# Kernel tuning notes

Measured on AMD Instinct MI355X. Metric: run time of the kernel, lower is better.

The kernel has to match this reference:

```python
import jax, jax.numpy as jnp
import numpy as np

K = 6
D_IN = 128
D_OUT = 128
N_COARSE = 4000
N_FINE = 40000


def setup_inputs() -> dict:
    key = jax.random.key(0)
    k1, k2, k3, k4, k5 = jax.random.split(key, 5)
    x_coarse = jax.random.normal(k1, (N_COARSE, D_IN), dtype=jnp.float32)
    pos_coarse = jax.random.uniform(k2, (N_COARSE, 3), dtype=jnp.float32)
    pos_fine = jax.random.uniform(k3, (N_FINE, 3), dtype=jnp.float32)
    # nnx.Linear params: lecun_normal kernel, zero bias (use small random for generality)
    W = jax.random.normal(k4, (D_IN, D_OUT), dtype=jnp.float32) / np.sqrt(D_IN)
    b = jax.random.normal(k5, (D_OUT,), dtype=jnp.float32) * 0.01
    return {"x_coarse": x_coarse, "pos_coarse": pos_coarse, "pos_fine": pos_fine, "W": W, "b": b}


def reference(x_coarse, pos_coarse, pos_fine, W, b):
    # dense pairwise L2 distances [Nf, Nc] (faithful to the original's full matrix)
    distances = jnp.linalg.norm(pos_fine[:, None, :] - pos_coarse[None, :, :], axis=-1)
    # full argsort then slice, matching the original (incl. tie-break order)
    knn_idx = jnp.argsort(distances, axis=1)[:, :K]        # [Nf, K]
    gathered = x_coarse[knn_idx]                            # [Nf, K, d_in]
    interp = jnp.mean(gathered, axis=1)                     # [Nf, d_in]
    return interp @ W + b                                   # [Nf, d_out]
```

## Files before the change

### kernel.cpp

```cpp
#include <hip/hip_runtime.h>
#include <cstdint>

#define NCOARSE 4000
#define NFINE   40000
#define DIM     128
#define GRES    8
#define CELLH   0.125f
#define FCAP    384
#define NB_B    128
#define NB_Y    125
#define NBUILD  (NB_B + NB_Y)

__device__ __forceinline__ uint64_t min64(uint64_t a, uint64_t b) { return a < b ? a : b; }
__device__ __forceinline__ uint64_t max64(uint64_t a, uint64_t b) { return a > b ? a : b; }
__device__ __forceinline__ int cell_coord(float x) {
    int c = (int)(x * 8.0f);
    return c < 0 ? 0 : (c > 7 ? 7 : c);
}

union BuildSM {
    uint16_t cellS[4096];
    float    xs[32][DIM];
};

__global__ __launch_bounds__(256) void k_build(const float* __restrict__ pc,
                                               const float* __restrict__ xc,
                                               const float* __restrict__ W,
                                               int*    __restrict__ nbrCnt,
                                               float4* __restrict__ flatC,
                                               float*  __restrict__ Y) {
    __shared__ BuildSM sm;
    const int bid = blockIdx.x, tid = threadIdx.x;

    if (bid < NB_B) {
        #pragma unroll
        for (int t = 0; t < 16; ++t) {
            const int idx = t * 256 + tid;
            uint16_t cv = 0xFFFF;
            if (idx < NCOARSE)
                cv = (uint16_t)((cell_coord(pc[3*idx+2]) << 6) |
                                (cell_coord(pc[3*idx+1]) << 3) |
                                 cell_coord(pc[3*idx]));
            sm.cellS[idx] = cv;
        }
        __syncthreads();
        const int wid = tid >> 6, lane = tid & 63;
        const int hc = bid * 4 + wid;
        const int hx = hc & 7, hy = (hc >> 3) & 7, hz = hc >> 6;
        const int bx0 = max(hx-1,0), bx1 = min(hx+1,7);
        const int by0 = max(hy-1,0), by1 = min(hy+1,7);
        const int bz0 = max(hz-1,0), bz1 = min(hz+1,7);
        int off = 0;
        for (int it = 0; it < 63; ++it) {
            const int j = it * 64 + lane;
            const uint16_t cid = sm.cellS[j];
            const int cx = cid & 7, cy = (cid >> 3) & 7, cz = cid >> 6;
            const bool in = (j < NCOARSE) && cx >= bx0 && cx <= bx1 &&
                            cy >= by0 && cy <= by1 && cz >= bz0 && cz <= bz1;
            const unsigned long long mask = __ballot(in);
            if (in) {
                const int d = off + (int)__popcll(mask & ((1ull << lane) - 1ull));
                if (d < FCAP)
                    flatC[hc * FCAP + d] =
                        make_float4(pc[3*j], pc[3*j+1], pc[3*j+2], __int_as_float(j));
            }
            off += (int)__popcll(mask);
        }
        if (lane == 0) nbrCnt[hc] = off;
    } else {
        const int g  = bid - NB_B;
        const int r0 = g * 32;
        #pragma unroll
        for (int t = 0; t < 4; ++t)
            reinterpret_cast<float4*>(sm.xs)[tid + t * 256] =
                reinterpret_cast<const float4*>(xc + r0 * DIM)[tid + t * 256];
        __syncthreads();
        const int rq = tid >> 5;
        const int jq = tid & 31;
        float acc[4][4];
        #pragma unroll
        for (int i = 0; i < 4; ++i)
            #pragma unroll
            for (int j = 0; j < 4; ++j) acc[i][j] = 0.f;
        #pragma unroll 2
        for (int k = 0; k < DIM; ++k) {
            const float4 wv = *reinterpret_cast<const float4*>(W + k * DIM + jq * 4);
            #pragma unroll
            for (int i = 0; i < 4; ++i) {
                const float a = sm.xs[rq + 8 * i][k];
                acc[i][0] += a * wv.x; acc[i][1] += a * wv.y;
                acc[i][2] += a * wv.z; acc[i][3] += a * wv.w;
            }
        }
        #pragma unroll
        for (int i = 0; i < 4; ++i)
            *reinterpret_cast<float4*>(Y + (r0 + rq + 8 * i) * DIM + jq * 4) =
                make_float4(acc[i][0], acc[i][1], acc[i][2], acc[i][3]);
    }
}

__device__ __forceinline__ void popmin_merge(const uint64_t own[7], uint64_t mg[7]) {
    uint64_t a0 = own[0], a1 = own[1], a2 = own[2], a3 = own[3],
             a4 = own[4], a5 = own[5], a6 = own[6];
    #pragma unroll
    for (int r = 0; r < 7; ++r) {
        uint64_t m = a0;
        m = min64(m, __shfl_xor((unsigned long long)m, 1));
        m = min64(m, __shfl_xor((unsigned long long)m, 2));
        m = min64(m, __shfl_xor((unsigned long long)m, 4));
        mg[r] = m;
        const bool win = (a0 == m);
        a0 = win ? a1 : a0;
        a1 = win ? a2 : a1;
        a2 = win ? a3 : a2;
        a3 = win ? a4 : a3;
        a4 = win ? a5 : a4;
        a5 = win ? a6 : a5;
        a6 = win ? ~0ull : a6;
    }
}

__device__ __forceinline__ bool done_check(uint64_t k7, float fx, float fy, float fz,
                                           int ix, int iy, int iz, int s) {
    const float d7 = __uint_as_float((uint32_t)(k7 >> 32));
    float clear = 1e30f;
    if (ix - s >= 0) clear = fminf(clear, __fsub_rn(fx, (float)(ix - s) * CELLH));
    if (ix + s <= 6) clear = fminf(clear, __fsub_rn((float)(ix + s + 1) * CELLH, fx));
    if (iy - s >= 0) clear = fminf(clear, __fsub_rn(fy, (float)(iy - s) * CELLH));
    if (iy + s <= 6) clear = fminf(clear, __fsub_rn((float)(iy + s + 1) * CELLH, fy));
    if (iz - s >= 0) clear = fminf(clear, __fsub_rn(fz, (float)(iz - s) * CELLH));
    if (iz + s <= 6) clear = fminf(clear, __fsub_rn((float)(iz + s + 1) * CELLH, fz));
    return d7 < clear * clear * 0.9999f;
}

#define INS(p) { \
    const float ddx = __fsub_rn(fx, (p).x); \
    const float ddy = __fsub_rn(fy, (p).y); \
    const float ddz = __fsub_rn(fz, (p).z); \
    const float d2  = __fadd_rn(__fadd_rn(__fmul_rn(ddx, ddx), __fmul_rn(ddy, ddy)), \
                                __fmul_rn(ddz, ddz)); \
    const uint64_t v = ((uint64_t)__float_as_uint(d2) << 32) | (uint32_t)__float_as_uint((p).w); \
    if (v < own[6]) { \
        own[6] = min64(own[6], max64(own[5], v)); \
        own[5] = min64(own[5], max64(own[4], v)); \
        own[4] = min64(own[4], max64(own[3], v)); \
        own[3] = min64(own[3], max64(own[2], v)); \
        own[2] = min64(own[2], max64(own[1], v)); \
        own[1] = min64(own[1], max64(own[0], v)); \
        own[0] = min64(own[0], v); \
    } }

#define BRUTE() { \
    _Pragma("unroll") \
    for (int r = 0; r < 7; ++r) own[r] = ~0ull; \
    for (int i = par; i < NCOARSE; i += 8) { \
        const float4 p = make_float4(pc[3*i], pc[3*i+1], pc[3*i+2], __int_as_float(i)); \
        INS(p) \
    } }

__global__ __launch_bounds__(256) void k_main(
    const float*  __restrict__ Y,
    const float*  __restrict__ bias,
    const int*    __restrict__ nbrCnt,
    const float4* __restrict__ flatC,
    const float*  __restrict__ pc,
    const float*  __restrict__ pf,
    float* __restrict__ out)
{
    const int tid = threadIdx.x;
    const int fl  = tid >> 3;
    const int par = tid & 7;
    const int f   = blockIdx.x * 32 + fl;

    const float fx = pf[3*f], fy = pf[3*f+1], fz = pf[3*f+2];
    const int ix = cell_coord(fx), iy = cell_coord(fy), iz = cell_coord(fz);
    const int cell = (iz << 6) | (iy << 3) | ix;

    const int total = nbrCnt[cell];

    uint64_t own[7];
    #pragma unroll
    for (int r = 0; r < 7; ++r) own[r] = ~0ull;
    uint64_t mg[7];

    if (total <= FCAP) {
        const float4* fpts = flatC + cell * FCAP;
        #pragma unroll 2
        for (int i = par; i < total; i += 8) { const float4 p = fpts[i]; INS(p) }
        popmin_merge(own, mg);
        if (!done_check(mg[6], fx, fy, fz, ix, iy, iz, 1)) {
            BRUTE();
            popmin_merge(own, mg);
        }
    } else {
        BRUTE();
        popmin_merge(own, mg);
    }

    int i5 = (int)(uint32_t)mg[5];
    {
        const int i6 = (int)(uint32_t)mg[6];
        const float d5 = sqrtf(__uint_as_float((uint32_t)(mg[5] >> 32)));
        const float d6 = sqrtf(__uint_as_float((uint32_t)(mg[6] >> 32)));
        if (d5 == d6 && i6 < i5) i5 = i6;
    }
    const int id0 = (int)(uint32_t)mg[0];
    const int id1 = (int)(uint32_t)mg[1];
    const int id2 = (int)(uint32_t)mg[2];
    const int id3 = (int)(uint32_t)mg[3];
    const int id4 = (int)(uint32_t)mg[4];
    const int id5 = i5;

    constexpr float inv6 = 1.0f / 6.0f;
    #pragma unroll
    for (int k = 0; k < 4; ++k) {
        const int q = (k * 8 + par) * 4;
        const float4 y0 = *reinterpret_cast<const float4*>(Y + id0 * DIM + q);
        const float4 y1 = *reinterpret_cast<const float4*>(Y + id1 * DIM + q);
        const float4 y2 = *reinterpret_cast<const float4*>(Y + id2 * DIM + q);
        const float4 y3 = *reinterpret_cast<const float4*>(Y + id3 * DIM + q);
        const float4 y4 = *reinterpret_cast<const float4*>(Y + id4 * DIM + q);
        const float4 y5 = *reinterpret_cast<const float4*>(Y + id5 * DIM + q);
        const float4 bv = *reinterpret_cast<const float4*>(bias + q);
        float4 o;
        o.x = (y0.x + y1.x + y2.x + y3.x + y4.x + y5.x) * inv6 + bv.x;
        o.y = (y0.y + y1.y + y2.y + y3.y + y4.y + y5.y) * inv6 + bv.y;
        o.z = (y0.z + y1.z + y2.z + y3.z + y4.z + y5.z) * inv6 + bv.z;
        o.w = (y0.w + y1.w + y2.w + y3.w + y4.w + y5.w) * inv6 + bv.w;
        *reinterpret_cast<float4*>(out + f * DIM + q) = o;
    }
}

extern "C" void kernel_launch(void* const* d_in, const int* in_sizes, int n_in,
                              void* d_out, int out_size, void* d_ws, size_t ws_size,
                              hipStream_t stream) {
    const float* xc = (const float*)d_in[0];
    const float* pc = (const float*)d_in[1];
    const float* pf = (const float*)d_in[2];
    const float* W  = (const float*)d_in[3];
    const float* b  = (const float*)d_in[4];
    float* out = (float*)d_out;

    int*    nbrCnt = (int*)d_ws;
    float4* flatC  = (float4*)((char*)d_ws + 4096);
    float*  Y      = (float*)((char*)d_ws + 3149824);

    k_build<<<dim3(NBUILD),      dim3(256), 0, stream>>>(pc, xc, W, nbrCnt, flatC, Y);
    k_main <<<dim3(NFINE / 32),  dim3(256), 0, stream>>>(Y, b, nbrCnt, flatC, pc, pf, out);
}
```

Measured before the change: 51.28 us.

## Sort neighbor candidates by distance to cell center and terminate scan early

The build kernel now sorts each cell's candidate list by distance to the cell center, using a shared-memory rank sort, and stores the sorted distances. The main kernel scans candidates in chunks of 64. It stops once the current 6th-best distance plus the query's offset from the cell center falls below the next candidate's center distance, which is a triangle-inequality bound. This cuts distance evaluations per query, but adds an O(m^2) rank sort to the build, extra shuffles, and a data-dependent loop exit.

Result: slower. 65.63 us (+28.0%).

```diff
diff --git a/kernel.cpp b/kernel.cpp
--- a/kernel.cpp
+++ b/kernel.cpp
@@ -19,8 +19,11 @@
 }
 
 union BuildSM {
-    uint16_t cellS[4096];
-    float    xs[32][DIM];
+    struct {
+        uint16_t cellS[4096];
+        uint64_t keys[4][FCAP];
+    } l;
+    float xs[32][DIM];
 };
 
 __global__ __launch_bounds__(256) void k_build(const float* __restrict__ pc,
@@ -28,6 +31,7 @@
                                                const float* __restrict__ W,
                                                int*    __restrict__ nbrCnt,
                                                float4* __restrict__ flatC,
+                                               float*  __restrict__ dsSorted,
                                                float*  __restrict__ Y) {
     __shared__ BuildSM sm;
     const int bid = blockIdx.x, tid = threadIdx.x;
@@ -41,7 +45,7 @@
                 cv = (uint16_t)((cell_coord(pc[3*idx+2]) << 6) |
                                 (cell_coord(pc[3*idx+1]) << 3) |
                                  cell_coord(pc[3*idx]));
-            sm.cellS[idx] = cv;
+            sm.l.cellS[idx] = cv;
         }
         __syncthreads();
         const int wid = tid >> 6, lane = tid & 63;
@@ -50,23 +54,43 @@
         const int bx0 = max(hx-1,0), bx1 = min(hx+1,7);
         const int by0 = max(hy-1,0), by1 = min(hy+1,7);
         const int bz0 = max(hz-1,0), bz1 = min(hz+1,7);
+        const float ccx = ((float)hx + 0.5f) * CELLH;
+        const float ccy = ((float)hy + 0.5f) * CELLH;
+        const float ccz = ((float)hz + 0.5f) * CELLH;
+
         int off = 0;
         for (int it = 0; it < 63; ++it) {
             const int j = it * 64 + lane;
-            const uint16_t cid = sm.cellS[j];
+            const uint16_t cid = sm.l.cellS[j];
             const int cx = cid & 7, cy = (cid >> 3) & 7, cz = cid >> 6;
             const bool in = (j < NCOARSE) && cx >= bx0 && cx <= bx1 &&
                             cy >= by0 && cy <= by1 && cz >= bz0 && cz <= bz1;
             const unsigned long long mask = __ballot(in);
             if (in) {
                 const int d = off + (int)__popcll(mask & ((1ull << lane) - 1ull));
-                if (d < FCAP)
-                    flatC[hc * FCAP + d] =
-                        make_float4(pc[3*j], pc[3*j+1], pc[3*j+2], __int_as_float(j));
+                if (d < FCAP) {
+                    const float dx = pc[3*j]   - ccx;
+                    const float dy = pc[3*j+1] - ccy;
+                    const float dz = pc[3*j+2] - ccz;
+                    const float d2c = dx*dx + dy*dy + dz*dz;
+                    sm.l.keys[wid][d] = ((uint64_t)__float_as_uint(d2c) << 32) | (uint32_t)j;
+                }
             }
             off += (int)__popcll(mask);
         }
         if (lane == 0) nbrCnt[hc] = off;
+        __syncthreads();
+
+        const int m = min(off, FCAP);
+        for (int l = lane; l < m; l += 64) {
+            const uint64_t k = sm.l.keys[wid][l];
+            int r = 0;
+            for (int q = 0; q < m; ++q) r += (sm.l.keys[wid][q] < k) ? 1 : 0;
+            const int j = (int)(uint32_t)k;
+            flatC[hc * FCAP + r] = make_float4(pc[3*j], pc[3*j+1], pc[3*j+2],
+                                               __int_as_float(j));
+            dsSorted[hc * FCAP + r] = sqrtf(__uint_as_float((uint32_t)(k >> 32)));
+        }
     } else {
         const int g  = bid - NB_B;
         const int r0 = g * 32;
@@ -163,6 +187,7 @@
     const float*  __restrict__ bias,
     const int*    __restrict__ nbrCnt,
     const float4* __restrict__ flatC,
+    const float*  __restrict__ dsSorted,
     const float*  __restrict__ pc,
     const float*  __restrict__ pf,
     float* __restrict__ out)
@@ -176,6 +201,12 @@
     const int ix = cell_coord(fx), iy = cell_coord(fy), iz = cell_coord(fz);
     const int cell = (iz << 6) | (iy << 3) | ix;
 
+    const float ccx = ((float)ix + 0.5f) * CELLH;
+    const float ccy = ((float)iy + 0.5f) * CELLH;
+    const float ccz = ((float)iz + 0.5f) * CELLH;
+    const float rfx = fx - ccx, rfy = fy - ccy, rfz = fz - ccz;
+    const float rf = sqrtf(rfx*rfx + rfy*rfy + rfz*rfz) * 1.0001f + 1e-6f;
+
     const int total = nbrCnt[cell];
 
     uint64_t own[7];
@@ -185,8 +216,21 @@
 
     if (total <= FCAP) {
         const float4* fpts = flatC + cell * FCAP;
-        #pragma unroll 2
-        for (int i = par; i < total; i += 8) { const float4 p = fpts[i]; INS(p) }
+        const float*  dss  = dsSorted + cell * FCAP;
+        int base = 0;
+        while (base < total) {
+            const int lim = min(base + 64, total);
+            for (int i = base + par; i < lim; i += 8) { const float4 p = fpts[i]; INS(p) }
+            base = lim;
+            if (base < total) {
+                uint64_t u7 = own[6];
+                u7 = min64(u7, __shfl_xor((unsigned long long)u7, 1));
+                u7 = min64(u7, __shfl_xor((unsigned long long)u7, 2));
+                u7 = min64(u7, __shfl_xor((unsigned long long)u7, 4));
+                const float d7u = sqrtf(__uint_as_float((uint32_t)(u7 >> 32)));
+                if ((d7u + rf) * 1.0002f < dss[base]) break;
+            }
+        }
         popmin_merge(own, mg);
         if (!done_check(mg[6], fx, fy, fz, ix, iy, iz, 1)) {
             BRUTE();
@@ -241,10 +285,13 @@
     const float* b  = (const float*)d_in[4];
     float* out = (float*)d_out;
 
-    int*    nbrCnt = (int*)d_ws;
-    float4* flatC  = (float4*)((char*)d_ws + 4096);
-    float*  Y      = (float*)((char*)d_ws + 3149824);
-
-    k_build<<<dim3(NBUILD),      dim3(256), 0, stream>>>(pc, xc, W, nbrCnt, flatC, Y);
-    k_main <<<dim3(NFINE / 32),  dim3(256), 0, stream>>>(Y, b, nbrCnt, flatC, pc, pf, out);
-}
+    int*    nbrCnt   = (int*)d_ws;
+    float4* flatC    = (float4*)((char*)d_ws + 4096);
+    float*  dsSorted = (float*)((char*)d_ws + 3149824);
+    float*  Y        = (float*)((char*)d_ws + 3936256);
+
+    k_build<<<dim3(NBUILD),     dim3(256), 0, stream>>>(pc, xc, W, nbrCnt, flatC,
+                                                        dsSorted, Y);
+    k_main <<<dim3(NFINE / 32), dim3(256), 0, stream>>>(Y, b, nbrCnt, flatC, dsSorted,
+                                                        pc, pf, out);
+}
```

## Use 16^3 subcell candidate lists pruned by kNN-radius bound

Applied to the files above, without the earlier changes.

Replaces the per-8^3-cell 27-neighborhood candidate lists (up to 384 points) with per-16^3-subcell lists. Each subcell's list holds only the coarse points within a radius derived from the 7th-nearest distance to the subcell center plus the subcell half-diagonal. The main kernel then scans a much shorter list per fine point and uses a triangle-inequality check against the stored radius to decide whether to fall back to brute force. This costs a heavier build kernel: 1024 build blocks each doing a wave-wide kNN and a filter pass. It also risks more brute-force fallbacks when the bound fails.

After: 48.72 us. 5.0% less time.

```diff
diff --git a/kernel.cpp b/kernel.cpp
--- a/kernel.cpp
+++ b/kernel.cpp
@@ -6,10 +6,13 @@
 #define DIM     128
 #define GRES    8
 #define CELLH   0.125f
-#define FCAP    384
-#define NB_B    128
+#define SUBH    0.0625f
+#define MCAP    384
+#define FCAP2   192
+#define NB_S    1024
 #define NB_Y    125
-#define NBUILD  (NB_B + NB_Y)
+#define NBUILD  (NB_S + NB_Y)
+#define LPP     8
 
 __device__ __forceinline__ uint64_t min64(uint64_t a, uint64_t b) { return a < b ? a : b; }
 __device__ __forceinline__ uint64_t max64(uint64_t a, uint64_t b) { return a > b ? a : b; }
@@ -17,22 +20,31 @@
     int c = (int)(x * 8.0f);
     return c < 0 ? 0 : (c > 7 ? 7 : c);
 }
+__device__ __forceinline__ int cell16(float x) {
+    int c = (int)(x * 16.0f);
+    return c < 0 ? 0 : (c > 15 ? 15 : c);
+}
 
 union BuildSM {
-    uint16_t cellS[4096];
-    float    xs[32][DIM];
+    struct {
+        uint16_t cellS[4096];
+        uint16_t memberIdx[MCAP];
+        int mcount, mflag;
+    } l;
+    float xs[32][DIM];
 };
 
 __global__ __launch_bounds__(256) void k_build(const float* __restrict__ pc,
                                                const float* __restrict__ xc,
                                                const float* __restrict__ W,
                                                int*    __restrict__ nbrCnt,
-                                               float4* __restrict__ flatC,
+                                               float*  __restrict__ Rarr,
+                                               float4* __restrict__ flatS,
                                                float*  __restrict__ Y) {
     __shared__ BuildSM sm;
     const int bid = blockIdx.x, tid = threadIdx.x;
 
-    if (bid < NB_B) {
+    if (bid < NB_S) {
         #pragma unroll
         for (int t = 0; t < 16; ++t) {
             const int idx = t * 256 + tid;
@@ -41,34 +53,120 @@
                 cv = (uint16_t)((cell_coord(pc[3*idx+2]) << 6) |
                                 (cell_coord(pc[3*idx+1]) << 3) |
                                  cell_coord(pc[3*idx]));
-            sm.cellS[idx] = cv;
+            sm.l.cellS[idx] = cv;
         }
         __syncthreads();
+
         const int wid = tid >> 6, lane = tid & 63;
-        const int hc = bid * 4 + wid;
-        const int hx = hc & 7, hy = (hc >> 3) & 7, hz = hc >> 6;
-        const int bx0 = max(hx-1,0), bx1 = min(hx+1,7);
-        const int by0 = max(hy-1,0), by1 = min(hy+1,7);
-        const int bz0 = max(hz-1,0), bz1 = min(hz+1,7);
-        int off = 0;
-        for (int it = 0; it < 63; ++it) {
-            const int j = it * 64 + lane;
-            const uint16_t cid = sm.cellS[j];
-            const int cx = cid & 7, cy = (cid >> 3) & 7, cz = cid >> 6;
-            const bool in = (j < NCOARSE) && cx >= bx0 && cx <= bx1 &&
-                            cy >= by0 && cy <= by1 && cz >= bz0 && cz <= bz1;
+        const int parent = bid >> 1;
+        const int px = parent & 7, py = (parent >> 3) & 7, pz = parent >> 6;
+        const int bx0 = max(px-1,0), bx1 = min(px+1,7);
+        const int by0 = max(py-1,0), by1 = min(py+1,7);
+        const int bz0 = max(pz-1,0), bz1 = min(pz+1,7);
+
+        if (wid == 0) {
+            int off = 0;
+            for (int it = 0; it < 63; ++it) {
+                const int j = it * 64 + lane;
+                const uint16_t cid = sm.l.cellS[j];
+                const int cx = cid & 7, cy = (cid >> 3) & 7, cz = cid >> 6;
+                const bool in = (j < NCOARSE) && cx >= bx0 && cx <= bx1 &&
+                                cy >= by0 && cy <= by1 && cz >= bz0 && cz <= bz1;
+                const unsigned long long mask = __ballot(in);
+                if (in) {
+                    const int d = off + (int)__popcll(mask & ((1ull << lane) - 1ull));
+                    if (d < MCAP) sm.l.memberIdx[d] = (uint16_t)j;
+                }
+                off += (int)__popcll(mask);
+            }
+            if (lane == 0) { sm.l.mcount = min(off, MCAP); sm.l.mflag = (off > MCAP); }
+        }
+        __syncthreads();
+
+        const int  mcount = sm.l.mcount;
+        const bool mflag  = sm.l.mflag != 0;
+
+        const int s  = (bid & 1) * 4 + wid;
+        const int gx = px * 2 + (s & 1);
+        const int gy = py * 2 + ((s >> 1) & 1);
+        const int gz = pz * 2 + (s >> 2);
+        const int SIDX = (gz << 8) | (gy << 4) | gx;
+        const float scx = ((float)gx + 0.5f) * SUBH;
+        const float scy = ((float)gy + 0.5f) * SUBH;
+        const float scz = ((float)gz + 0.5f) * SUBH;
+
+        uint64_t own[7];
+        #pragma unroll
+        for (int r = 0; r < 7; ++r) own[r] = ~0ull;
+        for (int i = lane; i < mcount; i += 64) {
+            const int j = (int)sm.l.memberIdx[i];
+            const float dx = pc[3*j]   - scx;
+            const float dy = pc[3*j+1] - scy;
+            const float dz = pc[3*j+2] - scz;
+            const float d2 = dx*dx + dy*dy + dz*dz;
+            const uint64_t v = ((uint64_t)__float_as_uint(d2) << 32) | (uint32_t)j;
+            if (v < own[6]) {
+                own[6] = min64(own[6], max64(own[5], v));
+                own[5] = min64(own[5], max64(own[4], v));
+                own[4] = min64(own[4], max64(own[3], v));
+                own[3] = min64(own[3], max64(own[2], v));
+                own[2] = min64(own[2], max64(own[1], v));
+                own[1] = min64(own[1], max64(own[0], v));
+                own[0] = min64(own[0], v);
+            }
+        }
+        uint64_t a0=own[0],a1=own[1],a2=own[2],a3=own[3],a4=own[4],a5=own[5],a6=own[6];
+        uint64_t d7key = ~0ull;
+        #pragma unroll
+        for (int r = 0; r < 7; ++r) {
+            uint64_t m = a0;
+            m = min64(m, __shfl_xor((unsigned long long)m, 1));
+            m = min64(m, __shfl_xor((unsigned long long)m, 2));
+            m = min64(m, __shfl_xor((unsigned long long)m, 4));
+            m = min64(m, __shfl_xor((unsigned long long)m, 8));
+            m = min64(m, __shfl_xor((unsigned long long)m, 16));
+            m = min64(m, __shfl_xor((unsigned long long)m, 32));
+            d7key = m;
+            const bool win = (a0 == m);
+            a0 = win ? a1 : a0; a1 = win ? a2 : a1; a2 = win ? a3 : a2;
+            a3 = win ? a4 : a3; a4 = win ? a5 : a4; a5 = win ? a6 : a5;
+            a6 = win ? ~0ull : a6;
+        }
+        const float d7c = sqrtf(__uint_as_float((uint32_t)(d7key >> 32)));
+
+        float clear = 1e30f;
+        if (bx0 > 0) clear = fminf(clear, scx - (float)bx0 * CELLH);
+        if (bx1 < 7) clear = fminf(clear, (float)(bx1+1) * CELLH - scx);
+        if (by0 > 0) clear = fminf(clear, scy - (float)by0 * CELLH);
+        if (by1 < 7) clear = fminf(clear, (float)(by1+1) * CELLH - scy);
+        if (bz0 > 0) clear = fminf(clear, scz - (float)bz0 * CELLH);
+        if (bz1 < 7) clear = fminf(clear, (float)(bz1+1) * CELLH - scz);
+
+        bool ok = (d7c < clear * 0.9999f) && !mflag && (mcount >= 7);
+        const float R  = d7c * 1.0001f + 0.1082533f + 1e-5f;
+        const float R2 = R * R;
+
+        int off2 = 0;
+        for (int i = lane; i < mcount; i += 64) {
+            const int j = (int)sm.l.memberIdx[i];
+            const float x = pc[3*j], y = pc[3*j+1], z = pc[3*j+2];
+            const float dx = x - scx, dy = y - scy, dz = z - scz;
+            const bool in = (dx*dx + dy*dy + dz*dz) <= R2;
             const unsigned long long mask = __ballot(in);
             if (in) {
-                const int d = off + (int)__popcll(mask & ((1ull << lane) - 1ull));
-                if (d < FCAP)
-                    flatC[hc * FCAP + d] =
-                        make_float4(pc[3*j], pc[3*j+1], pc[3*j+2], __int_as_float(j));
+                const int d = off2 + (int)__popcll(mask & ((1ull << lane) - 1ull));
+                if (d < FCAP2)
+                    flatS[SIDX * FCAP2 + d] = make_float4(x, y, z, __int_as_float(j));
             }
-            off += (int)__popcll(mask);
-        }
-        if (lane == 0) nbrCnt[hc] = off;
+            off2 += (int)__popcll(mask);
+        }
+        ok = ok && (off2 <= FCAP2) && (off2 >= 7);
+        if (lane == 0) {
+            nbrCnt[SIDX] = ok ? off2 : 0x40000000;
+            Rarr[SIDX]   = R;
+        }
     } else {
-        const int g  = bid - NB_B;
+        const int g  = bid - NB_S;
         const int r0 = g * 32;
         #pragma unroll
         for (int t = 0; t < 4; ++t)
@@ -110,27 +208,10 @@
         m = min64(m, __shfl_xor((unsigned long long)m, 4));
         mg[r] = m;
         const bool win = (a0 == m);
-        a0 = win ? a1 : a0;
-        a1 = win ? a2 : a1;
-        a2 = win ? a3 : a2;
-        a3 = win ? a4 : a3;
-        a4 = win ? a5 : a4;
-        a5 = win ? a6 : a5;
+        a0 = win ? a1 : a0; a1 = win ? a2 : a1; a2 = win ? a3 : a2;
+        a3 = win ? a4 : a3; a4 = win ? a5 : a4; a5 = win ? a6 : a5;
         a6 = win ? ~0ull : a6;
     }
-}
-
-__device__ __forceinline__ bool done_check(uint64_t k7, float fx, float fy, float fz,
-                                           int ix, int iy, int iz, int s) {
-    const float d7 = __uint_as_float((uint32_t)(k7 >> 32));
-    float clear = 1e30f;
-    if (ix - s >= 0) clear = fminf(clear, __fsub_rn(fx, (float)(ix - s) * CELLH));
-    if (ix + s <= 6) clear = fminf(clear, __fsub_rn((float)(ix + s + 1) * CELLH, fx));
-    if (iy - s >= 0) clear = fminf(clear, __fsub_rn(fy, (float)(iy - s) * CELLH));
-    if (iy + s <= 6) clear = fminf(clear, __fsub_rn((float)(iy + s + 1) * CELLH, fy));
-    if (iz - s >= 0) clear = fminf(clear, __fsub_rn(fz, (float)(iz - s) * CELLH));
-    if (iz + s <= 6) clear = fminf(clear, __fsub_rn((float)(iz + s + 1) * CELLH, fz));
-    return d7 < clear * clear * 0.9999f;
 }
 
 #define INS(p) { \
@@ -153,7 +234,7 @@
 #define BRUTE() { \
     _Pragma("unroll") \
     for (int r = 0; r < 7; ++r) own[r] = ~0ull; \
-    for (int i = par; i < NCOARSE; i += 8) { \
+    for (int i = par; i < NCOARSE; i += LPP) { \
         const float4 p = make_float4(pc[3*i], pc[3*i+1], pc[3*i+2], __int_as_float(i)); \
         INS(p) \
     } }
@@ -162,7 +243,8 @@
     const float*  __restrict__ Y,
     const float*  __restrict__ bias,
     const int*    __restrict__ nbrCnt,
-    const float4* __restrict__ flatC,
+    const float*  __restrict__ Rarr,
+    const float4* __restrict__ flatS,
     const float*  __restrict__ pc,
     const float*  __restrict__ pf,
     float* __restrict__ out)
@@ -173,22 +255,30 @@
     const int f   = blockIdx.x * 32 + fl;
 
     const float fx = pf[3*f], fy = pf[3*f+1], fz = pf[3*f+2];
-    const int ix = cell_coord(fx), iy = cell_coord(fy), iz = cell_coord(fz);
-    const int cell = (iz << 6) | (iy << 3) | ix;
-
-    const int total = nbrCnt[cell];
+    const int gx = cell16(fx), gy = cell16(fy), gz = cell16(fz);
+    const int SIDX = (gz << 8) | (gy << 4) | gx;
+
+    const float scx = ((float)gx + 0.5f) * SUBH;
+    const float scy = ((float)gy + 0.5f) * SUBH;
+    const float scz = ((float)gz + 0.5f) * SUBH;
+    const float ex = fx - scx, ey = fy - scy, ez = fz - scz;
+    const float dps = sqrtf(ex*ex + ey*ey + ez*ez) * 1.0001f + 1e-6f;
+
+    const int   n = nbrCnt[SIDX];
+    const float R = Rarr[SIDX];
 
     uint64_t own[7];
     #pragma unroll
     for (int r = 0; r < 7; ++r) own[r] = ~0ull;
     uint64_t mg[7];
 
-    if (total <= FCAP) {
-        const float4* fpts = flatC + cell * FCAP;
+    if (n <= FCAP2) {
+        const float4* fpts = flatS + SIDX * FCAP2;
         #pragma unroll 2
-        for (int i = par; i < total; i += 8) { const float4 p = fpts[i]; INS(p) }
+        for (int i = par; i < n; i += LPP) { const float4 p = fpts[i]; INS(p) }
         popmin_merge(own, mg);
-        if (!done_check(mg[6], fx, fy, fz, ix, iy, iz, 1)) {
+        const float d7u = sqrtf(__uint_as_float((uint32_t)(mg[6] >> 32)));
+        if (!((d7u + dps) * 1.0002f < R)) {
             BRUTE();
             popmin_merge(own, mg);
         }
@@ -242,9 +332,10 @@
     float* out = (float*)d_out;
 
     int*    nbrCnt = (int*)d_ws;
-    float4* flatC  = (float4*)((char*)d_ws + 4096);
-    float*  Y      = (float*)((char*)d_ws + 3149824);
-
-    k_build<<<dim3(NBUILD),      dim3(256), 0, stream>>>(pc, xc, W, nbrCnt, flatC, Y);
-    k_main <<<dim3(NFINE / 32),  dim3(256), 0, stream>>>(Y, b, nbrCnt, flatC, pc, pf, out);
-}
+    float*  Rarr   = (float*)((char*)d_ws + 16384);
+    float4* flatS  = (float4*)((char*)d_ws + 32768);
+    float*  Y      = (float*)((char*)d_ws + 12615680);
+
+    k_build<<<dim3(NBUILD),     dim3(256), 0, stream>>>(pc, xc, W, nbrCnt, Rarr, flatS, Y);
+    k_main <<<dim3(NFINE / 32), dim3(256), 0, stream>>>(Y, b, nbrCnt, Rarr, flatS, pc, pf, out);
+}
```
